# Kernel tuning notes

Hardware: AMD Instinct MI355X
Metric: run time of the kernel (lower is better)

## Reference

```python
import jax, jax.numpy as jnp
import numpy as np

# Hyperparameters from __init__
TEMPERATURE = 0.07
HARD_POS_W = 1.5
HARD_NEG_W = 2.0
THR_POS = 0.5
THR_NEG = 0.3
NEG_LOSS_W = 0.3

B, D, N_CLASSES = 8192, 256, 1024


def setup_inputs() -> dict:
    key = jax.random.key(0)
    kf, kl = jax.random.split(key)
    features = jax.random.normal(kf, (B, D), dtype=jnp.float32)
    labels = jax.random.randint(kl, (B,), 0, N_CLASSES, dtype=jnp.int32)
    return {"features": features, "labels": labels}


def reference(features, labels):
    b = features.shape[0]
    # L2-normalize features (F.normalize(dim=1))
    anchor = features / jnp.linalg.norm(features, axis=1, keepdims=True)
    sim = anchor @ anchor.T                      # [B, B] cosine similarity
    logits = sim / TEMPERATURE
    logits = logits - jax.lax.stop_gradient(jnp.max(logits, axis=1, keepdims=True))

    mask = (labels[:, None] == labels[None, :]).astype(logits.dtype)   # same-class
    logits_mask = 1.0 - jnp.eye(b, dtype=logits.dtype)                 # exclude self

    # W2ML weights: computed from detached similarities (torch used .item())
    sim_d = jax.lax.stop_gradient(sim)
    offdiag = logits_mask > 0
    is_pos = mask > 0
    hard_pos = is_pos & (sim_d < THR_POS) & offdiag
    pos_weights = jnp.where(
        hard_pos, 1.0 + (THR_POS - sim_d) / THR_POS * (HARD_POS_W - 1.0), 1.0)
    hard_neg = (~is_pos) & (sim_d > THR_NEG) & offdiag
    neg_weights = jnp.where(
        hard_neg, 1.0 + (sim_d - THR_NEG) / (1.0 - THR_NEG) * (HARD_NEG_W - 1.0), 1.0)

    # SupCon log-prob with self excluded from the denominator
    exp_logits = jnp.exp(logits) * logits_mask
    denom = jnp.sum(exp_logits, axis=1, keepdims=True)
    log_prob = logits - jnp.log(denom)

    pos_mask = mask * logits_mask
    pos_cnt = jnp.clip(jnp.sum(pos_mask, axis=1), 1.0, None)
    positive_loss = -jnp.mean(
        jnp.sum(pos_mask * pos_weights * log_prob, axis=1) / pos_cnt)

    # Negative term: weighted mean probability mass assigned to negatives
    neg_mask = (1.0 - mask) * logits_mask
    neg_cnt = jnp.clip(jnp.sum(neg_mask, axis=1), 1.0, None)
    prob = exp_logits / denom
    negative_loss = jnp.mean(
        jnp.sum(neg_mask * neg_weights * prob, axis=1) / neg_cnt)

    return positive_loss + NEG_LOSS_W * negative_loss
```

## Files before the change

### kernel.cpp

```cpp
#include <hip/hip_runtime.h>

#define BSZ  8192
#define DDIM 256
#define BM 128
#define BN 128
#define NT   64
#define NTRI (NT * (NT + 1) / 2)

typedef float f32x4 __attribute__((ext_vector_type(4)));
typedef short bf16x8 __attribute__((ext_vector_type(8)));

__device__ __forceinline__ unsigned short f32_to_bf16(float f) {
    unsigned int u = __float_as_uint(f);
    u += 0x7fffu + ((u >> 16) & 1u);
    return (unsigned short)(u >> 16);
}

#define K_E1   20.60992915555662f
#define K_E2  -20.60992915555662f
#define K_INVT 14.285714285714286f
#define K_N1   1.4285714285714286f
#define K_N2   0.5714285714285714f

__global__ __launch_bounds__(256) void norm_kernel(const float* __restrict__ feat,
                                                   unsigned short* __restrict__ anchorT,
                                                   float* __restrict__ posAcc) {
    if (blockIdx.x < 128) posAcc[blockIdx.x * 256 + threadIdx.x] = 0.0f;
    const int wid  = threadIdx.x >> 6;
    const int lane = threadIdx.x & 63;
    const int row  = blockIdx.x * 4 + wid;
    const float4 v = ((const float4*)(feat + (size_t)row * DDIM))[lane];
    float ss = v.x * v.x + v.y * v.y + v.z * v.z + v.w * v.w;
    #pragma unroll
    for (int off = 32; off > 0; off >>= 1) ss += __shfl_xor(ss, off, 64);
    const float inv = rsqrtf(ss);
    ushort4 o;
    o.x = f32_to_bf16(v.x * inv);
    o.y = f32_to_bf16(v.y * inv);
    o.z = f32_to_bf16(v.z * inv);
    o.w = f32_to_bf16(v.w * inv);
    const int C    = lane >> 3;
    const int tile = C * 512 + (row >> 4);
    const int l16  = (row & 15) + (((lane >> 1) & 3) << 4);
    *(ushort4*)(anchorT + (size_t)tile * 512 + l16 * 8 + (lane & 1) * 4) = o;
}

__device__ __forceinline__ void gload_lds16(const unsigned short* g, unsigned short* l) {
    __builtin_amdgcn_global_load_lds(
        (const __attribute__((address_space(1))) void*)g,
        (__attribute__((address_space(3))) void*)l, 16, 0, 0);
}

__global__ __launch_bounds__(256) void simloss_kernel(
    const unsigned short* __restrict__ anchorT,
    const int* __restrict__ labels,
    float* __restrict__ part,
    float* __restrict__ posAcc)
{
    __shared__ __align__(16) unsigned short As[16 * 512];
    __shared__ __align__(16) unsigned short Bs[16 * 512];
    __shared__ float rowDT[2][BM][2];
    __shared__ float colDT[2][BN][2];
    __shared__ int rowLab[BM];
    __shared__ int colLab[BN];

    const int t = blockIdx.x;
    const int off1 = 136, off2 = 392, off3 = 648, off4 = 904, off5 = 1040,
              off6 = 1296, off7 = 1552, off8 = 1688, off9 = 1944;
    int b = (t >= off1) + (t >= off2) + (t >= off3) + (t >= off4) + (t >= off5)
          + (t >= off6) + (t >= off7) + (t >= off8) + (t >= off9);
    int si, sj, r0;
    switch (b) {
        case 0: si = 0; sj = 0; r0 = 0;    break;
        case 1: si = 0; sj = 1; r0 = off1; break;
        case 2: si = 0; sj = 2; r0 = off2; break;
        case 3: si = 0; sj = 3; r0 = off3; break;
        case 4: si = 1; sj = 1; r0 = off4; break;
        case 5: si = 1; sj = 2; r0 = off5; break;
        case 6: si = 1; sj = 3; r0 = off6; break;
        case 7: si = 2; sj = 2; r0 = off7; break;
        case 8: si = 2; sj = 3; r0 = off8; break;
        default: si = 3; sj = 3; r0 = off9; break;
    }
    const int rr = t - r0;
    int il, jl;
    if (si == sj) {
        il = 0;
        #pragma unroll
        for (int q = 1; q < 16; q++) if (rr >= (16 * q - (q * (q - 1)) / 2)) il = q;
        jl = il + (rr - (16 * il - (il * (il - 1)) / 2));
    } else {
        il = rr >> 4;
        jl = rr & 15;
    }
    const int It = si * 16 + il;
    const int Jt = sj * 16 + jl;
    const bool diag = (It == Jt);
    const int I0 = It * BM, J0 = Jt * BN;

    const int tid  = threadIdx.x;
    const int wid  = tid >> 6;
    const int lane = tid & 63;
    const int waveM = (wid >> 1) * 64;
    const int waveN = (wid & 1) * 64;
    const int wm4 = waveM >> 4;
    const int wn4 = waveN >> 4;
    const int cl = lane & 15;
    const int rg = lane >> 4;
    const bool dwave = diag && (waveM == waveN);

    if (tid < BM) rowLab[tid] = labels[I0 + tid];
    else          colLab[tid - BM] = labels[J0 + tid - BM];

    f32x4 c_acc[4][4];
    #pragma unroll
    for (int a = 0; a < 4; a++)
        #pragma unroll
        for (int bq = 0; bq < 4; bq++)
            c_acc[a][bq] = (f32x4){0.f, 0.f, 0.f, 0.f};

    const int laneOff = lane * 8;

    for (int kc = 0; kc < 4; kc++) {
        const int C0 = kc * 2;
        #pragma unroll
        for (int q = 0; q < 4; q++) {
            const int chunk = wid * 4 + q;
            const int cq = chunk >> 3;
            const int Rq = chunk & 7;
            const size_t at = ((size_t)(C0 + cq) * 512 + It * 8 + Rq) * 512;
            const size_t bt = ((size_t)(C0 + cq) * 512 + Jt * 8 + Rq) * 512;
            gload_lds16(anchorT + at + laneOff, &As[chunk * 512]);
            gload_lds16(anchorT + bt + laneOff, &Bs[chunk * 512]);
        }
        __syncthreads();
        #pragma unroll
        for (int ks = 0; ks < 2; ks++) {
            const unsigned short* ab = &As[(ks * 8 + wm4) * 512 + laneOff];
            const unsigned short* bb = &Bs[(ks * 8 + wn4) * 512 + laneOff];
            const bf16x8 a0 = *(const bf16x8*)(ab);
            const bf16x8 a1 = *(const bf16x8*)(ab + 512);
            const bf16x8 a2 = *(const bf16x8*)(ab + 1024);
            const bf16x8 a3 = *(const bf16x8*)(ab + 1536);
            const bf16x8 b0 = *(const bf16x8*)(bb);
            const bf16x8 b1 = *(const bf16x8*)(bb + 512);
            const bf16x8 b2 = *(const bf16x8*)(bb + 1024);
            const bf16x8 b3 = *(const bf16x8*)(bb + 1536);
            c_acc[0][0] = __builtin_amdgcn_mfma_f32_16x16x32_bf16(a0, b0, c_acc[0][0], 0, 0, 0);
            c_acc[0][1] = __builtin_amdgcn_mfma_f32_16x16x32_bf16(a0, b1, c_acc[0][1], 0, 0, 0);
            c_acc[0][2] = __builtin_amdgcn_mfma_f32_16x16x32_bf16(a0, b2, c_acc[0][2], 0, 0, 0);
            c_acc[0][3] = __builtin_amdgcn_mfma_f32_16x16x32_bf16(a0, b3, c_acc[0][3], 0, 0, 0);
            c_acc[1][0] = __builtin_amdgcn_mfma_f32_16x16x32_bf16(a1, b0, c_acc[1][0], 0, 0, 0);
            c_acc[1][1] = __builtin_amdgcn_mfma_f32_16x16x32_bf16(a1, b1, c_acc[1][1], 0, 0, 0);
            c_acc[1][2] = __builtin_amdgcn_mfma_f32_16x16x32_bf16(a1, b2, c_acc[1][2], 0, 0, 0);
            c_acc[1][3] = __builtin_amdgcn_mfma_f32_16x16x32_bf16(a1, b3, c_acc[1][3], 0, 0, 0);
            c_acc[2][0] = __builtin_amdgcn_mfma_f32_16x16x32_bf16(a2, b0, c_acc[2][0], 0, 0, 0);
            c_acc[2][1] = __builtin_amdgcn_mfma_f32_16x16x32_bf16(a2, b1, c_acc[2][1], 0, 0, 0);
            c_acc[2][2] = __builtin_amdgcn_mfma_f32_16x16x32_bf16(a2, b2, c_acc[2][2], 0, 0, 0);
            c_acc[2][3] = __builtin_amdgcn_mfma_f32_16x16x32_bf16(a2, b3, c_acc[2][3], 0, 0, 0);
            c_acc[3][0] = __builtin_amdgcn_mfma_f32_16x16x32_bf16(a3, b0, c_acc[3][0], 0, 0, 0);
            c_acc[3][1] = __builtin_amdgcn_mfma_f32_16x16x32_bf16(a3, b1, c_acc[3][1], 0, 0, 0);
            c_acc[3][2] = __builtin_amdgcn_mfma_f32_16x16x32_bf16(a3, b2, c_acc[3][2], 0, 0, 0);
            c_acc[3][3] = __builtin_amdgcn_mfma_f32_16x16x32_bf16(a3, b3, c_acc[3][3], 0, 0, 0);
        }
        __syncthreads();
    }

    int ljr[4], gjr[4];
    #pragma unroll
    for (int fc = 0; fc < 4; fc++) {
        const int cidx = waveN + fc * 16 + cl;
        ljr[fc] = colLab[cidx];
        gjr[fc] = J0 + cidx;
    }
    float cd[4] = {0.f, 0.f, 0.f, 0.f}, ct[4] = {0.f, 0.f, 0.f, 0.f};

    #pragma unroll
    for (int fr = 0; fr < 4; fr++) {
        float rd[4] = {0.f, 0.f, 0.f, 0.f}, rt[4] = {0.f, 0.f, 0.f, 0.f};
        int li[4], gi[4];
        #pragma unroll
        for (int r = 0; r < 4; r++) {
            const int ridx = waveM + fr * 16 + rg * 4 + r;
            li[r] = rowLab[ridx];
            gi[r] = I0 + ridx;
        }
        #pragma unroll
        for (int fc = 0; fc < 4; fc++) {
            const int lj = ljr[fc];
            const f32x4 c = c_acc[fr][fc];
            #pragma unroll
            for (int r = 0; r < 4; r++) {
                const float s = c[r];
                const bool self = diag && (fr == fc) && dwave && ((rg * 4 + r) == cl);
                const float e  = self ? 0.f : exp2f(fmaf(s, K_E1, K_E2));
                const float wn = fmaxf(fmaf(s, K_N1, K_N2), 1.0f);
                const float we = wn * e;
                rd[r] += e;  rt[r] += we;
                if (!diag) { cd[fc] += e; ct[fc] += we; }
                if (li[r] == lj && !self) {
                    const float wp = fmaxf(1.5f - s, 1.0f);
                    const float slp = fmaf(s, K_INVT, -K_INVT) * wp;
                    float* pi = posAcc + (size_t)gi[r] * 4;
                    atomicAdd(pi + 0, slp);
                    atomicAdd(pi + 1, wp);
                    atomicAdd(pi + 2, we);
                    atomicAdd(pi + 3, 1.0f);
                    if (!diag) {
                        float* pj = posAcc + (size_t)gjr[fc] * 4;
                        atomicAdd(pj + 0, slp);
                        atomicAdd(pj + 1, wp);
                        atomicAdd(pj + 2, we);
                        atomicAdd(pj + 3, 1.0f);
                    }
                }
            }
        }
        #pragma unroll
        for (int r = 0; r < 4; r++) {
            #pragma unroll
            for (int off = 1; off < 16; off <<= 1) {
                rd[r] += __shfl_xor(rd[r], off, 64);
                rt[r] += __shfl_xor(rt[r], off, 64);
            }
        }
        if (cl == 0) {
            const int wh = waveN >> 6;
            #pragma unroll
            for (int r = 0; r < 4; r++) {
                const int row = waveM + fr * 16 + rg * 4 + r;
                rowDT[wh][row][0] = rd[r];
                rowDT[wh][row][1] = rt[r];
            }
        }
    }
    if (!diag) {
        #pragma unroll
        for (int fc = 0; fc < 4; fc++) {
            cd[fc] += __shfl_xor(cd[fc], 16, 64);
            cd[fc] += __shfl_xor(cd[fc], 32, 64);
            ct[fc] += __shfl_xor(ct[fc], 16, 64);
            ct[fc] += __shfl_xor(ct[fc], 32, 64);
        }
        if (rg == 0) {
            const int wmh = waveM >> 6;
            #pragma unroll
            for (int fc = 0; fc < 4; fc++) {
                const int col = waveN + fc * 16 + cl;
                colDT[wmh][col][0] = cd[fc];
                colDT[wmh][col][1] = ct[fc];
            }
        }
    }

    __syncthreads();
    if (tid < BM) {
        float2 v;
        v.x = rowDT[0][tid][0] + rowDT[1][tid][0];
        v.y = rowDT[0][tid][1] + rowDT[1][tid][1];
        ((float2*)part)[(size_t)Jt * BSZ + I0 + tid] = v;
    } else if (!diag) {
        const int c = tid - BM;
        float2 v;
        v.x = colDT[0][c][0] + colDT[1][c][0];
        v.y = colDT[0][c][1] + colDT[1][c][1];
        ((float2*)part)[(size_t)It * BSZ + J0 + c] = v;
    }
}

__global__ __launch_bounds__(256) void reduce_kernel(
    const float* __restrict__ part, const float* __restrict__ posAcc,
    double* __restrict__ partial)
{
    const int i = blockIdx.x * 256 + threadIdx.x;
    float dsum = 0.f, T2 = 0.f;
    const float2* p2 = (const float2*)part;
    #pragma unroll 8
    for (int j = 0; j < NT; j++) {
        const float2 v = p2[(size_t)j * BSZ + i];
        dsum += v.x; T2 += v.y;
    }
    const float4 pa = ((const float4*)posAcc)[i];
    const float s1 = pa.x, w1 = pa.y, s2 = T2 - pa.z, cnt = pa.w;
    const float pc = fmaxf(cnt, 1.0f);
    const float nc = fmaxf(8191.0f - cnt, 1.0f);
    const float ld = logf(dsum);
    const double pos_i = (double)((s1 - ld * w1) / pc);
    const double neg_i = (double)((s2 / dsum) / nc);

    __shared__ double sp[256], sn[256];
    sp[threadIdx.x] = pos_i; sn[threadIdx.x] = neg_i;
    __syncthreads();
    for (int s = 128; s > 0; s >>= 1) {
        if (threadIdx.x < s) {
            sp[threadIdx.x] += sp[threadIdx.x + s];
            sn[threadIdx.x] += sn[threadIdx.x + s];
        }
        __syncthreads();
    }
    if (threadIdx.x == 0) {
        partial[blockIdx.x * 2 + 0] = sp[0];
        partial[blockIdx.x * 2 + 1] = sn[0];
    }
}

__global__ __launch_bounds__(64) void final_kernel(const double* __restrict__ partial,
                                                   float* __restrict__ out) {
    const int lane = threadIdx.x;
    double p = 0.0, n = 0.0;
    if (lane < 32) { p = partial[lane * 2 + 0]; n = partial[lane * 2 + 1]; }
    #pragma unroll
    for (int o = 32; o > 0; o >>= 1) { p += __shfl_xor(p, o, 64); n += __shfl_xor(n, o, 64); }
    if (lane == 0) out[0] = (float)(-p / (double)BSZ + 0.3 * (n / (double)BSZ));
}

extern "C" void kernel_launch(void* const* d_in, const int* in_sizes, int n_in,
                              void* d_out, int out_size, void* d_ws, size_t ws_size,
                              hipStream_t stream) {
    const float* feat = (const float*)d_in[0];
    const int* labels = (const int*)d_in[1];
    float* out = (float*)d_out;

    char* ws = (char*)d_ws;
    unsigned short* anchorT = (unsigned short*)ws;
    const size_t anchorBytes = (size_t)BSZ * DDIM * sizeof(unsigned short);
    float* part = (float*)(ws + anchorBytes);
    const size_t partBytes = (size_t)NT * BSZ * 2 * sizeof(float);
    float* posAcc = (float*)(ws + anchorBytes + partBytes);
    const size_t posBytes = (size_t)BSZ * 4 * sizeof(float);
    double* partial = (double*)(ws + anchorBytes + partBytes + posBytes);

    norm_kernel<<<BSZ / 4, 256, 0, stream>>>(feat, anchorT, posAcc);
    simloss_kernel<<<NTRI, 256, 0, stream>>>(anchorT, labels, part, posAcc);
    reduce_kernel<<<BSZ / 256, 256, 0, stream>>>(part, posAcc, partial);
    final_kernel<<<1, 64, 0, stream>>>(partial, out);
}
```

Before: 122.4 us.

## Make simloss persistent over four tiles with double-buffered LDS prefetch and fused final reduction

The sim/loss kernel now launches 520 blocks that each process four triangle tiles, double-buffering the A/B LDS tiles so the global-to-LDS loads for the next k-chunk or next tile overlap the MFMA work. Row and column partial sums go straight to global memory per wave half, which removes the shared-memory staging and the final block barrier, at the cost of doubling the partial buffer the reduce reads. The norm kernel stages 64 rows in LDS so it can write contiguous 16-byte chunks. The final kernel is folded into the reduce through a last-block atomic counter, saving one launch.

```diff
diff --git a/kernel.cpp b/kernel.cpp
--- a/kernel.cpp
+++ b/kernel.cpp
@@ -6,6 +6,7 @@
 #define BN 128
 #define NT   64
 #define NTRI (NT * (NT + 1) / 2)
+#define NBLK 520
 
 typedef float f32x4 __attribute__((ext_vector_type(4)));
 typedef short bf16x8 __attribute__((ext_vector_type(8)));
@@ -22,49 +23,7 @@
 #define K_N1   1.4285714285714286f
 #define K_N2   0.5714285714285714f
 
-__global__ __launch_bounds__(256) void norm_kernel(const float* __restrict__ feat,
-                                                   unsigned short* __restrict__ anchorT,
-                                                   float* __restrict__ posAcc) {
-    if (blockIdx.x < 128) posAcc[blockIdx.x * 256 + threadIdx.x] = 0.0f;
-    const int wid  = threadIdx.x >> 6;
-    const int lane = threadIdx.x & 63;
-    const int row  = blockIdx.x * 4 + wid;
-    const float4 v = ((const float4*)(feat + (size_t)row * DDIM))[lane];
-    float ss = v.x * v.x + v.y * v.y + v.z * v.z + v.w * v.w;
-    #pragma unroll
-    for (int off = 32; off > 0; off >>= 1) ss += __shfl_xor(ss, off, 64);
-    const float inv = rsqrtf(ss);
-    ushort4 o;
-    o.x = f32_to_bf16(v.x * inv);
-    o.y = f32_to_bf16(v.y * inv);
-    o.z = f32_to_bf16(v.z * inv);
-    o.w = f32_to_bf16(v.w * inv);
-    const int C    = lane >> 3;
-    const int tile = C * 512 + (row >> 4);
-    const int l16  = (row & 15) + (((lane >> 1) & 3) << 4);
-    *(ushort4*)(anchorT + (size_t)tile * 512 + l16 * 8 + (lane & 1) * 4) = o;
-}
-
-__device__ __forceinline__ void gload_lds16(const unsigned short* g, unsigned short* l) {
-    __builtin_amdgcn_global_load_lds(
-        (const __attribute__((address_space(1))) void*)g,
-        (__attribute__((address_space(3))) void*)l, 16, 0, 0);
-}
-
-__global__ __launch_bounds__(256) void simloss_kernel(
-    const unsigned short* __restrict__ anchorT,
-    const int* __restrict__ labels,
-    float* __restrict__ part,
-    float* __restrict__ posAcc)
-{
-    __shared__ __align__(16) unsigned short As[16 * 512];
-    __shared__ __align__(16) unsigned short Bs[16 * 512];
-    __shared__ float rowDT[2][BM][2];
-    __shared__ float colDT[2][BN][2];
-    __shared__ int rowLab[BM];
-    __shared__ int colLab[BN];
-
-    const int t = blockIdx.x;
+__device__ __forceinline__ void decode_tile(int t, int& It, int& Jt) {
     const int off1 = 136, off2 = 392, off3 = 648, off4 = 904, off5 = 1040,
               off6 = 1296, off7 = 1552, off8 = 1688, off9 = 1944;
     int b = (t >= off1) + (t >= off2) + (t >= off3) + (t >= off4) + (t >= off5)
@@ -93,11 +52,68 @@
         il = rr >> 4;
         jl = rr & 15;
     }
-    const int It = si * 16 + il;
-    const int Jt = sj * 16 + jl;
-    const bool diag = (It == Jt);
-    const int I0 = It * BM, J0 = Jt * BN;
-
+    It = si * 16 + il;
+    Jt = sj * 16 + jl;
+}
+
+__global__ __launch_bounds__(256) void norm_kernel(const float* __restrict__ feat,
+                                                   unsigned short* __restrict__ anchorT,
+                                                   float* __restrict__ posAcc,
+                                                   unsigned int* __restrict__ counter) {
+    __shared__ __align__(16) unsigned short img[32 * 512];
+    const int tid  = threadIdx.x;
+    const int wid  = tid >> 6;
+    const int lane = tid & 63;
+    const int R0   = blockIdx.x * 64;
+
+    posAcc[blockIdx.x * 256 + tid] = 0.0f;
+    if (blockIdx.x == 0 && tid == 0) *counter = 0u;
+
+    #pragma unroll
+    for (int it = 0; it < 16; it++) {
+        const int row = R0 + it * 4 + wid;
+        const float4 v = ((const float4*)(feat + (size_t)row * DDIM))[lane];
+        float ss = v.x * v.x + v.y * v.y + v.z * v.z + v.w * v.w;
+        #pragma unroll
+        for (int off = 32; off > 0; off >>= 1) ss += __shfl_xor(ss, off, 64);
+        const float inv = rsqrtf(ss);
+        ushort4 o;
+        o.x = f32_to_bf16(v.x * inv);
+        o.y = f32_to_bf16(v.y * inv);
+        o.z = f32_to_bf16(v.z * inv);
+        o.w = f32_to_bf16(v.w * inv);
+        const int C    = lane >> 3;
+        const int c    = C * 4 + ((row >> 4) & 3);
+        const int l16  = (row & 15) + (((lane >> 1) & 3) << 4);
+        *(ushort4*)(&img[c * 512 + l16 * 8 + (lane & 1) * 4]) = o;
+    }
+    __syncthreads();
+    #pragma unroll
+    for (int p = 0; p < 8; p++) {
+        const int c = p * 4 + wid;
+        const int T = (c >> 2) * 512 + (R0 >> 4) + (c & 3);
+        *(bf16x8*)(anchorT + (size_t)T * 512 + lane * 8) = *(const bf16x8*)(&img[c * 512 + lane * 8]);
+    }
+}
+
+__device__ __forceinline__ void gload_lds16(const unsigned short* g, unsigned short* l) {
+    __builtin_amdgcn_global_load_lds(
+        (const __attribute__((address_space(1))) void*)g,
+        (__attribute__((address_space(3))) void*)l, 16, 0, 0);
+}
+
+__global__ __launch_bounds__(256) void simloss_kernel(
+    const unsigned short* __restrict__ anchorT,
+    const int* __restrict__ labels,
+    float* __restrict__ part,
+    float* __restrict__ posAcc)
+{
+    __shared__ __align__(16) unsigned short As[2][16 * 512];
+    __shared__ __align__(16) unsigned short Bs[2][16 * 512];
+    __shared__ int rowLab[2][BM];
+    __shared__ int colLab[2][BN];
+
+    const int p    = blockIdx.x;
     const int tid  = threadIdx.x;
     const int wid  = tid >> 6;
     const int lane = tid & 63;
@@ -107,176 +123,196 @@
     const int wn4 = waveN >> 4;
     const int cl = lane & 15;
     const int rg = lane >> 4;
-    const bool dwave = diag && (waveM == waveN);
-
-    if (tid < BM) rowLab[tid] = labels[I0 + tid];
-    else          colLab[tid - BM] = labels[J0 + tid - BM];
-
-    f32x4 c_acc[4][4];
-    #pragma unroll
-    for (int a = 0; a < 4; a++)
-        #pragma unroll
-        for (int bq = 0; bq < 4; bq++)
-            c_acc[a][bq] = (f32x4){0.f, 0.f, 0.f, 0.f};
-
     const int laneOff = lane * 8;
 
-    for (int kc = 0; kc < 4; kc++) {
-        const int C0 = kc * 2;
-        #pragma unroll
-        for (int q = 0; q < 4; q++) {
-            const int chunk = wid * 4 + q;
-            const int cq = chunk >> 3;
-            const int Rq = chunk & 7;
-            const size_t at = ((size_t)(C0 + cq) * 512 + It * 8 + Rq) * 512;
-            const size_t bt = ((size_t)(C0 + cq) * 512 + Jt * 8 + Rq) * 512;
-            gload_lds16(anchorT + at + laneOff, &As[chunk * 512]);
-            gload_lds16(anchorT + bt + laneOff, &Bs[chunk * 512]);
-        }
-        __syncthreads();
-        #pragma unroll
-        for (int ks = 0; ks < 2; ks++) {
-            const unsigned short* ab = &As[(ks * 8 + wm4) * 512 + laneOff];
-            const unsigned short* bb = &Bs[(ks * 8 + wn4) * 512 + laneOff];
-            const bf16x8 a0 = *(const bf16x8*)(ab);
-            const bf16x8 a1 = *(const bf16x8*)(ab + 512);
-            const bf16x8 a2 = *(const bf16x8*)(ab + 1024);
-            const bf16x8 a3 = *(const bf16x8*)(ab + 1536);
-            const bf16x8 b0 = *(const bf16x8*)(bb);
-            const bf16x8 b1 = *(const bf16x8*)(bb + 512);
-            const bf16x8 b2 = *(const bf16x8*)(bb + 1024);
-            const bf16x8 b3 = *(const bf16x8*)(bb + 1536);
-            c_acc[0][0] = __builtin_amdgcn_mfma_f32_16x16x32_bf16(a0, b0, c_acc[0][0], 0, 0, 0);
-            c_acc[0][1] = __builtin_amdgcn_mfma_f32_16x16x32_bf16(a0, b1, c_acc[0][1], 0, 0, 0);
-            c_acc[0][2] = __builtin_amdgcn_mfma_f32_16x16x32_bf16(a0, b2, c_acc[0][2], 0, 0, 0);
-            c_acc[0][3] = __builtin_amdgcn_mfma_f32_16x16x32_bf16(a0, b3, c_acc[0][3], 0, 0, 0);
-            c_acc[1][0] = __builtin_amdgcn_mfma_f32_16x16x32_bf16(a1, b0, c_acc[1][0], 0, 0, 0);
-            c_acc[1][1] = __builtin_amdgcn_mfma_f32_16x16x32_bf16(a1, b1, c_acc[1][1], 0, 0, 0);
-            c_acc[1][2] = __builtin_amdgcn_mfma_f32_16x16x32_bf16(a1, b2, c_acc[1][2], 0, 0, 0);
-            c_acc[1][3] = __builtin_amdgcn_mfma_f32_16x16x32_bf16(a1, b3, c_acc[1][3], 0, 0, 0);
-            c_acc[2][0] = __builtin_amdgcn_mfma_f32_16x16x32_bf16(a2, b0, c_acc[2][0], 0, 0, 0);
-            c_acc[2][1] = __builtin_amdgcn_mfma_f32_16x16x32_bf16(a2, b1, c_acc[2][1], 0, 0, 0);
-            c_acc[2][2] = __builtin_amdgcn_mfma_f32_16x16x32_bf16(a2, b2, c_acc[2][2], 0, 0, 0);
-            c_acc[2][3] = __builtin_amdgcn_mfma_f32_16x16x32_bf16(a2, b3, c_acc[2][3], 0, 0, 0);
-            c_acc[3][0] = __builtin_amdgcn_mfma_f32_16x16x32_bf16(a3, b0, c_acc[3][0], 0, 0, 0);
-            c_acc[3][1] = __builtin_amdgcn_mfma_f32_16x16x32_bf16(a3, b1, c_acc[3][1], 0, 0, 0);
-            c_acc[3][2] = __builtin_amdgcn_mfma_f32_16x16x32_bf16(a3, b2, c_acc[3][2], 0, 0, 0);
-            c_acc[3][3] = __builtin_amdgcn_mfma_f32_16x16x32_bf16(a3, b3, c_acc[3][3], 0, 0, 0);
-        }
-        __syncthreads();
-    }
-
-    int ljr[4], gjr[4];
-    #pragma unroll
-    for (int fc = 0; fc < 4; fc++) {
-        const int cidx = waveN + fc * 16 + cl;
-        ljr[fc] = colLab[cidx];
-        gjr[fc] = J0 + cidx;
-    }
-    float cd[4] = {0.f, 0.f, 0.f, 0.f}, ct[4] = {0.f, 0.f, 0.f, 0.f};
-
-    #pragma unroll
-    for (int fr = 0; fr < 4; fr++) {
-        float rd[4] = {0.f, 0.f, 0.f, 0.f}, rt[4] = {0.f, 0.f, 0.f, 0.f};
-        int li[4], gi[4];
-        #pragma unroll
-        for (int r = 0; r < 4; r++) {
-            const int ridx = waveM + fr * 16 + rg * 4 + r;
-            li[r] = rowLab[ridx];
-            gi[r] = I0 + ridx;
-        }
+    int It, Jt;
+    decode_tile(p * 4, It, Jt);
+
+    #define STAGE(ItX, JtX, kcX, slotX)                                              \
+        do {                                                                          \
+            const int C0s = (kcX) * 2;                                                \
+            _Pragma("unroll")                                                         \
+            for (int q = 0; q < 4; q++) {                                             \
+                const int chunk = wid * 4 + q;                                        \
+                const int cq = chunk >> 3;                                            \
+                const int Rq = chunk & 7;                                             \
+                const size_t at = ((size_t)(C0s + cq) * 512 + (ItX) * 8 + Rq) * 512;  \
+                const size_t bt = ((size_t)(C0s + cq) * 512 + (JtX) * 8 + Rq) * 512;  \
+                gload_lds16(anchorT + at + laneOff, &As[slotX][chunk * 512]);         \
+                gload_lds16(anchorT + bt + laneOff, &Bs[slotX][chunk * 512]);         \
+            }                                                                         \
+        } while (0)
+
+    #define WRLAB(ItX, JtX, slotX)                                                    \
+        do {                                                                          \
+            if (tid < BM) rowLab[slotX][tid] = labels[(ItX) * BM + tid];              \
+            else          colLab[slotX][tid - BM] = labels[(JtX) * BN + tid - BM];    \
+        } while (0)
+
+    STAGE(It, Jt, 0, 0);
+    WRLAB(It, Jt, 0);
+
+    #pragma unroll 1
+    for (int ti = 0; ti < 4; ++ti) {
+        const bool diag  = (It == Jt);
+        const bool dwave = diag && (waveM == waveN);
+        const int I0 = It * BM, J0 = Jt * BN;
+        const int ls = ti & 1;
+
+        int Itn = It, Jtn = Jt;
+        if (ti < 3) decode_tile(p * 4 + ti + 1, Itn, Jtn);
+
+        f32x4 c_acc[4][4];
+        #pragma unroll
+        for (int a = 0; a < 4; a++)
+            #pragma unroll
+            for (int bq = 0; bq < 4; bq++)
+                c_acc[a][bq] = (f32x4){0.f, 0.f, 0.f, 0.f};
+
+        #pragma unroll
+        for (int kc = 0; kc < 4; ++kc) {
+            __syncthreads();
+            if (kc < 3) {
+                STAGE(It, Jt, kc + 1, (kc + 1) & 1);
+            } else if (ti < 3) {
+                STAGE(Itn, Jtn, 0, 0);
+                WRLAB(Itn, Jtn, (ti + 1) & 1);
+            }
+            const int s = kc & 1;
+            #pragma unroll
+            for (int ks = 0; ks < 2; ks++) {
+                const unsigned short* ab = &As[s][(ks * 8 + wm4) * 512 + laneOff];
+                const unsigned short* bb = &Bs[s][(ks * 8 + wn4) * 512 + laneOff];
+                const bf16x8 a0 = *(const bf16x8*)(ab);
+                const bf16x8 a1 = *(const bf16x8*)(ab + 512);
+                const bf16x8 a2 = *(const bf16x8*)(ab + 1024);
+                const bf16x8 a3 = *(const bf16x8*)(ab + 1536);
+                const bf16x8 b0 = *(const bf16x8*)(bb);
+                const bf16x8 b1 = *(const bf16x8*)(bb + 512);
+                const bf16x8 b2 = *(const bf16x8*)(bb + 1024);
+                const bf16x8 b3 = *(const bf16x8*)(bb + 1536);
+                c_acc[0][0] = __builtin_amdgcn_mfma_f32_16x16x32_bf16(a0, b0, c_acc[0][0], 0, 0, 0);
+                c_acc[0][1] = __builtin_amdgcn_mfma_f32_16x16x32_bf16(a0, b1, c_acc[0][1], 0, 0, 0);
+                c_acc[0][2] = __builtin_amdgcn_mfma_f32_16x16x32_bf16(a0, b2, c_acc[0][2], 0, 0, 0);
+                c_acc[0][3] = __builtin_amdgcn_mfma_f32_16x16x32_bf16(a0, b3, c_acc[0][3], 0, 0, 0);
+                c_acc[1][0] = __builtin_amdgcn_mfma_f32_16x16x32_bf16(a1, b0, c_acc[1][0], 0, 0, 0);
+                c_acc[1][1] = __builtin_amdgcn_mfma_f32_16x16x32_bf16(a1, b1, c_acc[1][1], 0, 0, 0);
+                c_acc[1][2] = __builtin_amdgcn_mfma_f32_16x16x32_bf16(a1, b2, c_acc[1][2], 0, 0, 0);
+                c_acc[1][3] = __builtin_amdgcn_mfma_f32_16x16x32_bf16(a1, b3, c_acc[1][3], 0, 0, 0);
+                c_acc[2][0] = __builtin_amdgcn_mfma_f32_16x16x32_bf16(a2, b0, c_acc[2][0], 0, 0, 0);
+                c_acc[2][1] = __builtin_amdgcn_mfma_f32_16x16x32_bf16(a2, b1, c_acc[2][1], 0, 0, 0);
+                c_acc[2][2] = __builtin_amdgcn_mfma_f32_16x16x32_bf16(a2, b2, c_acc[2][2], 0, 0, 0);
+                c_acc[2][3] = __builtin_amdgcn_mfma_f32_16x16x32_bf16(a2, b3, c_acc[2][3], 0, 0, 0);
+                c_acc[3][0] = __builtin_amdgcn_mfma_f32_16x16x32_bf16(a3, b0, c_acc[3][0], 0, 0, 0);
+                c_acc[3][1] = __builtin_amdgcn_mfma_f32_16x16x32_bf16(a3, b1, c_acc[3][1], 0, 0, 0);
+                c_acc[3][2] = __builtin_amdgcn_mfma_f32_16x16x32_bf16(a3, b2, c_acc[3][2], 0, 0, 0);
+                c_acc[3][3] = __builtin_amdgcn_mfma_f32_16x16x32_bf16(a3, b3, c_acc[3][3], 0, 0, 0);
+            }
+        }
+
+        int ljr[4], gjr[4];
         #pragma unroll
         for (int fc = 0; fc < 4; fc++) {
-            const int lj = ljr[fc];
-            const f32x4 c = c_acc[fr][fc];
+            const int cidx = waveN + fc * 16 + cl;
+            ljr[fc] = colLab[ls][cidx];
+            gjr[fc] = J0 + cidx;
+        }
+        float cd[4] = {0.f, 0.f, 0.f, 0.f}, ct[4] = {0.f, 0.f, 0.f, 0.f};
+
+        #pragma unroll
+        for (int fr = 0; fr < 4; fr++) {
+            float rd[4] = {0.f, 0.f, 0.f, 0.f}, rt[4] = {0.f, 0.f, 0.f, 0.f};
+            int li[4], gi[4];
             #pragma unroll
             for (int r = 0; r < 4; r++) {
-                const float s = c[r];
-                const bool self = diag && (fr == fc) && dwave && ((rg * 4 + r) == cl);
-                const float e  = self ? 0.f : exp2f(fmaf(s, K_E1, K_E2));
-                const float wn = fmaxf(fmaf(s, K_N1, K_N2), 1.0f);
-                const float we = wn * e;
-                rd[r] += e;  rt[r] += we;
-                if (!diag) { cd[fc] += e; ct[fc] += we; }
-                if (li[r] == lj && !self) {
-                    const float wp = fmaxf(1.5f - s, 1.0f);
-                    const float slp = fmaf(s, K_INVT, -K_INVT) * wp;
-                    float* pi = posAcc + (size_t)gi[r] * 4;
-                    atomicAdd(pi + 0, slp);
-                    atomicAdd(pi + 1, wp);
-                    atomicAdd(pi + 2, we);
-                    atomicAdd(pi + 3, 1.0f);
-                    if (!diag) {
-                        float* pj = posAcc + (size_t)gjr[fc] * 4;
-                        atomicAdd(pj + 0, slp);
-                        atomicAdd(pj + 1, wp);
-                        atomicAdd(pj + 2, we);
-                        atomicAdd(pj + 3, 1.0f);
+                const int ridx = waveM + fr * 16 + rg * 4 + r;
+                li[r] = rowLab[ls][ridx];
+                gi[r] = I0 + ridx;
+            }
+            #pragma unroll
+            for (int fc = 0; fc < 4; fc++) {
+                const int lj = ljr[fc];
+                const f32x4 c = c_acc[fr][fc];
+                #pragma unroll
+                for (int r = 0; r < 4; r++) {
+                    const float s = c[r];
+                    const bool self = diag && (fr == fc) && dwave && ((rg * 4 + r) == cl);
+                    const float e  = self ? 0.f : exp2f(fmaf(s, K_E1, K_E2));
+                    const float wn = fmaxf(fmaf(s, K_N1, K_N2), 1.0f);
+                    const float we = wn * e;
+                    rd[r] += e;  rt[r] += we;
+                    if (!diag) { cd[fc] += e; ct[fc] += we; }
+                    if (li[r] == lj && !self) {
+                        const float wp = fmaxf(1.5f - s, 1.0f);
+                        const float slp = fmaf(s, K_INVT, -K_INVT) * wp;
+                        float* pi = posAcc + (size_t)gi[r] * 4;
+                        atomicAdd(pi + 0, slp);
+                        atomicAdd(pi + 1, wp);
+                        atomicAdd(pi + 2, we);
+                        atomicAdd(pi + 3, 1.0f);
+                        if (!diag) {
+                            float* pj = posAcc + (size_t)gjr[fc] * 4;
+                            atomicAdd(pj + 0, slp);
+                            atomicAdd(pj + 1, wp);
+                            atomicAdd(pj + 2, we);
+                            atomicAdd(pj + 3, 1.0f);
+                        }
                     }
                 }
             }
-        }
-        #pragma unroll
-        for (int r = 0; r < 4; r++) {
-            #pragma unroll
-            for (int off = 1; off < 16; off <<= 1) {
-                rd[r] += __shfl_xor(rd[r], off, 64);
-                rt[r] += __shfl_xor(rt[r], off, 64);
-            }
-        }
-        if (cl == 0) {
-            const int wh = waveN >> 6;
             #pragma unroll
             for (int r = 0; r < 4; r++) {
-                const int row = waveM + fr * 16 + rg * 4 + r;
-                rowDT[wh][row][0] = rd[r];
-                rowDT[wh][row][1] = rt[r];
-            }
-        }
-    }
-    if (!diag) {
-        #pragma unroll
-        for (int fc = 0; fc < 4; fc++) {
-            cd[fc] += __shfl_xor(cd[fc], 16, 64);
-            cd[fc] += __shfl_xor(cd[fc], 32, 64);
-            ct[fc] += __shfl_xor(ct[fc], 16, 64);
-            ct[fc] += __shfl_xor(ct[fc], 32, 64);
-        }
-        if (rg == 0) {
-            const int wmh = waveM >> 6;
+                #pragma unroll
+                for (int off = 1; off < 16; off <<= 1) {
+                    rd[r] += __shfl_xor(rd[r], off, 64);
+                    rt[r] += __shfl_xor(rt[r], off, 64);
+                }
+            }
+            if (cl == 0) {
+                const int wh = waveN >> 6;
+                float2* dst = (float2*)part + ((size_t)(Jt * 2 + wh)) * BSZ + I0 + waveM + fr * 16 + rg * 4;
+                #pragma unroll
+                for (int r = 0; r < 4; r++) {
+                    float2 v; v.x = rd[r]; v.y = rt[r];
+                    dst[r] = v;
+                }
+            }
+        }
+        if (!diag) {
             #pragma unroll
             for (int fc = 0; fc < 4; fc++) {
-                const int col = waveN + fc * 16 + cl;
-                colDT[wmh][col][0] = cd[fc];
-                colDT[wmh][col][1] = ct[fc];
-            }
-        }
-    }
-
-    __syncthreads();
-    if (tid < BM) {
-        float2 v;
-        v.x = rowDT[0][tid][0] + rowDT[1][tid][0];
-        v.y = rowDT[0][tid][1] + rowDT[1][tid][1];
-        ((float2*)part)[(size_t)Jt * BSZ + I0 + tid] = v;
-    } else if (!diag) {
-        const int c = tid - BM;
-        float2 v;
-        v.x = colDT[0][c][0] + colDT[1][c][0];
-        v.y = colDT[0][c][1] + colDT[1][c][1];
-        ((float2*)part)[(size_t)It * BSZ + J0 + c] = v;
-    }
-}
-
-__global__ __launch_bounds__(256) void reduce_kernel(
+                cd[fc] += __shfl_xor(cd[fc], 16, 64);
+                cd[fc] += __shfl_xor(cd[fc], 32, 64);
+                ct[fc] += __shfl_xor(ct[fc], 16, 64);
+                ct[fc] += __shfl_xor(ct[fc], 32, 64);
+            }
+            if (rg == 0) {
+                const int wmh = waveM >> 6;
+                float2* dst = (float2*)part + ((size_t)(It * 2 + wmh)) * BSZ + J0 + waveN + cl;
+                #pragma unroll
+                for (int fc = 0; fc < 4; fc++) {
+                    float2 v; v.x = cd[fc]; v.y = ct[fc];
+                    dst[fc * 16] = v;
+                }
+            }
+        }
+
+        It = Itn; Jt = Jtn;
+    }
+    #undef STAGE
+    #undef WRLAB
+}
+
+__global__ __launch_bounds__(256) void reduce_final_kernel(
     const float* __restrict__ part, const float* __restrict__ posAcc,
-    double* __restrict__ partial)
+    double* __restrict__ partial, unsigned int* __restrict__ counter,
+    float* __restrict__ out)
 {
     const int i = blockIdx.x * 256 + threadIdx.x;
     float dsum = 0.f, T2 = 0.f;
     const float2* p2 = (const float2*)part;
-    #pragma unroll 8
-    for (int j = 0; j < NT; j++) {
+    #pragma unroll 4
+    for (int j = 0; j < NT * 2; j++) {
         const float2 v = p2[(size_t)j * BSZ + i];
         dsum += v.x; T2 += v.y;
     }
@@ -298,20 +334,27 @@
         }
         __syncthreads();
     }
+    __shared__ bool amLast;
     if (threadIdx.x == 0) {
         partial[blockIdx.x * 2 + 0] = sp[0];
         partial[blockIdx.x * 2 + 1] = sn[0];
-    }
-}
-
-__global__ __launch_bounds__(64) void final_kernel(const double* __restrict__ partial,
-                                                   float* __restrict__ out) {
-    const int lane = threadIdx.x;
-    double p = 0.0, n = 0.0;
-    if (lane < 32) { p = partial[lane * 2 + 0]; n = partial[lane * 2 + 1]; }
-    #pragma unroll
-    for (int o = 32; o > 0; o >>= 1) { p += __shfl_xor(p, o, 64); n += __shfl_xor(n, o, 64); }
-    if (lane == 0) out[0] = (float)(-p / (double)BSZ + 0.3 * (n / (double)BSZ));
+        __threadfence();
+        amLast = (atomicAdd(counter, 1u) == 31u);
+    }
+    __syncthreads();
+    if (amLast) {
+        __threadfence();
+        const int lane = threadIdx.x;
+        double p = 0.0, n = 0.0;
+        if (lane < 32) {
+            volatile double* vp = (volatile double*)partial;
+            p = vp[lane * 2 + 0];
+            n = vp[lane * 2 + 1];
+        }
+        #pragma unroll
+        for (int o = 32; o > 0; o >>= 1) { p += __shfl_xor(p, o, 64); n += __shfl_xor(n, o, 64); }
+        if (lane == 0) out[0] = (float)(-p / (double)BSZ + 0.3 * (n / (double)BSZ));
+    }
 }
 
 extern "C" void kernel_launch(void* const* d_in, const int* in_sizes, int n_in,
@@ -325,13 +368,13 @@
     unsigned short* anchorT = (unsigned short*)ws;
     const size_t anchorBytes = (size_t)BSZ * DDIM * sizeof(unsigned short);
     float* part = (float*)(ws + anchorBytes);
-    const size_t partBytes = (size_t)NT * BSZ * 2 * sizeof(float);
+    const size_t partBytes = (size_t)NT * 2 * BSZ * 2 * sizeof(float);
     float* posAcc = (float*)(ws + anchorBytes + partBytes);
     const size_t posBytes = (size_t)BSZ * 4 * sizeof(float);
     double* partial = (double*)(ws + anchorBytes + partBytes + posBytes);
-
-    norm_kernel<<<BSZ / 4, 256, 0, stream>>>(feat, anchorT, posAcc);
-    simloss_kernel<<<NTRI, 256, 0, stream>>>(anchorT, labels, part, posAcc);
-    reduce_kernel<<<BSZ / 256, 256, 0, stream>>>(part, posAcc, partial);
-    final_kernel<<<1, 64, 0, stream>>>(partial, out);
-}
+    unsigned int* counter = (unsigned int*)(ws + anchorBytes + partBytes + posBytes + 512);
+
+    norm_kernel<<<BSZ / 64, 256, 0, stream>>>(feat, anchorT, posAcc, counter);
+    simloss_kernel<<<NBLK, 256, 0, stream>>>(anchorT, labels, part, posAcc);
+    reduce_final_kernel<<<BSZ / 256, 256, 0, stream>>>(part, posAcc, partial, counter, out);
+}
```

Result: slower. 182.5 us (+49.2%).

## Fuse reduce and final kernels, stage norm output in LDS, shrink GEMM K-chunk

Applied to the files above, without the earlier changes.

The norm kernel now handles 16 rows per block and writes whole 1KB tiles through LDS with coalesced 16-byte stores, and it also resets a completion counter. The simloss GEMM loads K in eight single-chunk steps with precomputed pointers and half the LDS, which may raise occupancy but doubles the barrier count. The reduce and final kernels merge into one kernel that uses more blocks and shuffle reductions, and the last block to finish does the final sum via an atomic counter. This removes one launch at the cost of threadfence and atomic overhead.

```diff
diff --git a/kernel.cpp b/kernel.cpp
--- a/kernel.cpp
+++ b/kernel.cpp
@@ -22,49 +22,7 @@
 #define K_N1   1.4285714285714286f
 #define K_N2   0.5714285714285714f
 
-__global__ __launch_bounds__(256) void norm_kernel(const float* __restrict__ feat,
-                                                   unsigned short* __restrict__ anchorT,
-                                                   float* __restrict__ posAcc) {
-    if (blockIdx.x < 128) posAcc[blockIdx.x * 256 + threadIdx.x] = 0.0f;
-    const int wid  = threadIdx.x >> 6;
-    const int lane = threadIdx.x & 63;
-    const int row  = blockIdx.x * 4 + wid;
-    const float4 v = ((const float4*)(feat + (size_t)row * DDIM))[lane];
-    float ss = v.x * v.x + v.y * v.y + v.z * v.z + v.w * v.w;
-    #pragma unroll
-    for (int off = 32; off > 0; off >>= 1) ss += __shfl_xor(ss, off, 64);
-    const float inv = rsqrtf(ss);
-    ushort4 o;
-    o.x = f32_to_bf16(v.x * inv);
-    o.y = f32_to_bf16(v.y * inv);
-    o.z = f32_to_bf16(v.z * inv);
-    o.w = f32_to_bf16(v.w * inv);
-    const int C    = lane >> 3;
-    const int tile = C * 512 + (row >> 4);
-    const int l16  = (row & 15) + (((lane >> 1) & 3) << 4);
-    *(ushort4*)(anchorT + (size_t)tile * 512 + l16 * 8 + (lane & 1) * 4) = o;
-}
-
-__device__ __forceinline__ void gload_lds16(const unsigned short* g, unsigned short* l) {
-    __builtin_amdgcn_global_load_lds(
-        (const __attribute__((address_space(1))) void*)g,
-        (__attribute__((address_space(3))) void*)l, 16, 0, 0);
-}
-
-__global__ __launch_bounds__(256) void simloss_kernel(
-    const unsigned short* __restrict__ anchorT,
-    const int* __restrict__ labels,
-    float* __restrict__ part,
-    float* __restrict__ posAcc)
-{
-    __shared__ __align__(16) unsigned short As[16 * 512];
-    __shared__ __align__(16) unsigned short Bs[16 * 512];
-    __shared__ float rowDT[2][BM][2];
-    __shared__ float colDT[2][BN][2];
-    __shared__ int rowLab[BM];
-    __shared__ int colLab[BN];
-
-    const int t = blockIdx.x;
+__device__ __forceinline__ void decode_tile(int t, int& It, int& Jt) {
     const int off1 = 136, off2 = 392, off3 = 648, off4 = 904, off5 = 1040,
               off6 = 1296, off7 = 1552, off8 = 1688, off9 = 1944;
     int b = (t >= off1) + (t >= off2) + (t >= off3) + (t >= off4) + (t >= off5)
@@ -93,8 +51,71 @@
         il = rr >> 4;
         jl = rr & 15;
     }
-    const int It = si * 16 + il;
-    const int Jt = sj * 16 + jl;
+    It = si * 16 + il;
+    Jt = sj * 16 + jl;
+}
+
+__global__ __launch_bounds__(256) void norm_kernel(const float* __restrict__ feat,
+                                                   unsigned short* __restrict__ anchorT,
+                                                   float* __restrict__ posAcc,
+                                                   unsigned int* __restrict__ counter) {
+    __shared__ __align__(16) unsigned short img[8 * 512];
+    const int tid  = threadIdx.x;
+    const int wid  = tid >> 6;
+    const int lane = tid & 63;
+    const int R    = blockIdx.x;
+    const int R0   = R * 16;
+
+    if (tid < 64) posAcc[blockIdx.x * 64 + tid] = 0.0f;
+    if (blockIdx.x == 0 && tid == 0) *counter = 0u;
+
+    #pragma unroll
+    for (int it = 0; it < 4; it++) {
+        const int row = R0 + it * 4 + wid;
+        const float4 v = ((const float4*)(feat + (size_t)row * DDIM))[lane];
+        float ss = v.x * v.x + v.y * v.y + v.z * v.z + v.w * v.w;
+        #pragma unroll
+        for (int off = 32; off > 0; off >>= 1) ss += __shfl_xor(ss, off, 64);
+        const float inv = rsqrtf(ss);
+        ushort4 o;
+        o.x = f32_to_bf16(v.x * inv);
+        o.y = f32_to_bf16(v.y * inv);
+        o.z = f32_to_bf16(v.z * inv);
+        o.w = f32_to_bf16(v.w * inv);
+        const int C    = lane >> 3;
+        const int l16  = (row & 15) + (((lane >> 1) & 3) << 4);
+        *(ushort4*)(&img[C * 512 + l16 * 8 + (lane & 1) * 4]) = o;
+    }
+    __syncthreads();
+    #pragma unroll
+    for (int p = 0; p < 2; p++) {
+        const int c = p * 4 + wid;
+        *(bf16x8*)(anchorT + ((size_t)(c * 512 + R)) * 512 + lane * 8) =
+            *(const bf16x8*)(&img[c * 512 + lane * 8]);
+    }
+}
+
+__device__ __forceinline__ void gload_lds16(const unsigned short* g, unsigned short* l) {
+    __builtin_amdgcn_global_load_lds(
+        (const __attribute__((address_space(1))) void*)g,
+        (__attribute__((address_space(3))) void*)l, 16, 0, 0);
+}
+
+__global__ __launch_bounds__(256) void simloss_kernel(
+    const unsigned short* __restrict__ anchorT,
+    const int* __restrict__ labels,
+    float* __restrict__ part,
+    float* __restrict__ posAcc)
+{
+    __shared__ __align__(16) unsigned short As[8 * 512];
+    __shared__ __align__(16) unsigned short Bs[8 * 512];
+    __shared__ float rowDT[2][BM][2];
+    __shared__ float colDT[2][BN][2];
+    __shared__ int rowLab[BM];
+    __shared__ int colLab[BN];
+
+    int It, Jt;
+    decode_tile(blockIdx.x, It, Jt);
     const bool diag = (It == Jt);
     const int I0 = It * BM, J0 = Jt * BN;
 
@@ -108,60 +129,58 @@
     const int cl = lane & 15;
     const int rg = lane >> 4;
     const bool dwave = diag && (waveM == waveN);
+    const int laneOff = lane * 8;
 
     if (tid < BM) rowLab[tid] = labels[I0 + tid];
     else          colLab[tid - BM] = labels[J0 + tid - BM];
 
-    f32x4 c_acc[4][4];
+    const unsigned short* aG0 = anchorT + ((size_t)(It * 8 + wid)) * 512 + laneOff;
+    const unsigned short* aG1 = aG0 + (size_t)4 * 512;
+    const unsigned short* bG0 = anchorT + ((size_t)(Jt * 8 + wid)) * 512 + laneOff;
+    const unsigned short* bG1 = bG0 + (size_t)4 * 512;
+
+    f32x4 acc[4][4];
     #pragma unroll
     for (int a = 0; a < 4; a++)
         #pragma unroll
         for (int bq = 0; bq < 4; bq++)
-            c_acc[a][bq] = (f32x4){0.f, 0.f, 0.f, 0.f};
-
-    const int laneOff = lane * 8;
-
-    for (int kc = 0; kc < 4; kc++) {
-        const int C0 = kc * 2;
-        #pragma unroll
-        for (int q = 0; q < 4; q++) {
-            const int chunk = wid * 4 + q;
-            const int cq = chunk >> 3;
-            const int Rq = chunk & 7;
-            const size_t at = ((size_t)(C0 + cq) * 512 + It * 8 + Rq) * 512;
-            const size_t bt = ((size_t)(C0 + cq) * 512 + Jt * 8 + Rq) * 512;
-            gload_lds16(anchorT + at + laneOff, &As[chunk * 512]);
-            gload_lds16(anchorT + bt + laneOff, &Bs[chunk * 512]);
-        }
+            acc[a][bq] = (f32x4){0.f, 0.f, 0.f, 0.f};
+
+    #pragma unroll
+    for (int kc = 0; kc < 8; kc++) {
+        const size_t adv = (size_t)kc * (512 * 512);
+        gload_lds16(aG0 + adv, &As[wid * 512]);
+        gload_lds16(aG1 + adv, &As[(4 + wid) * 512]);
+        gload_lds16(bG0 + adv, &Bs[wid * 512]);
+        gload_lds16(bG1 + adv, &Bs[(4 + wid) * 512]);
         __syncthreads();
-        #pragma unroll
-        for (int ks = 0; ks < 2; ks++) {
-            const unsigned short* ab = &As[(ks * 8 + wm4) * 512 + laneOff];
-            const unsigned short* bb = &Bs[(ks * 8 + wn4) * 512 + laneOff];
-            const bf16x8 a0 = *(const bf16x8*)(ab);
-            const bf16x8 a1 = *(const bf16x8*)(ab + 512);
-            const bf16x8 a2 = *(const bf16x8*)(ab + 1024);
-            const bf16x8 a3 = *(const bf16x8*)(ab + 1536);
-            const bf16x8 b0 = *(const bf16x8*)(bb);
-            const bf16x8 b1 = *(const bf16x8*)(bb + 512);
-            const bf16x8 b2 = *(const bf16x8*)(bb + 1024);
-            const bf16x8 b3 = *(const bf16x8*)(bb + 1536);
-            c_acc[0][0] = __builtin_amdgcn_mfma_f32_16x16x32_bf16(a0, b0, c_acc[0][0], 0, 0, 0);
-            c_acc[0][1] = __builtin_amdgcn_mfma_f32_16x16x32_bf16(a0, b1, c_acc[0][1], 0, 0, 0);
-            c_acc[0][2] = __builtin_amdgcn_mfma_f32_16x16x32_bf16(a0, b2, c_acc[0][2], 0, 0, 0);
-            c_acc[0][3] = __builtin_amdgcn_mfma_f32_16x16x32_bf16(a0, b3, c_acc[0][3], 0, 0, 0);
-            c_acc[1][0] = __builtin_amdgcn_mfma_f32_16x16x32_bf16(a1, b0, c_acc[1][0], 0, 0, 0);
-            c_acc[1][1] = __builtin_amdgcn_mfma_f32_16x16x32_bf16(a1, b1, c_acc[1][1], 0, 0, 0);
-            c_acc[1][2] = __builtin_amdgcn_mfma_f32_16x16x32_bf16(a1, b2, c_acc[1][2], 0, 0, 0);
-            c_acc[1][3] = __builtin_amdgcn_mfma_f32_16x16x32_bf16(a1, b3, c_acc[1][3], 0, 0, 0);
-            c_acc[2][0] = __builtin_amdgcn_mfma_f32_16x16x32_bf16(a2, b0, c_acc[2][0], 0, 0, 0);
-            c_acc[2][1] = __builtin_amdgcn_mfma_f32_16x16x32_bf16(a2, b1, c_acc[2][1], 0, 0, 0);
-            c_acc[2][2] = __builtin_amdgcn_mfma_f32_16x16x32_bf16(a2, b2, c_acc[2][2], 0, 0, 0);
-            c_acc[2][3] = __builtin_amdgcn_mfma_f32_16x16x32_bf16(a2, b3, c_acc[2][3], 0, 0, 0);
-            c_acc[3][0] = __builtin_amdgcn_mfma_f32_16x16x32_bf16(a3, b0, c_acc[3][0], 0, 0, 0);
-            c_acc[3][1] = __builtin_amdgcn_mfma_f32_16x16x32_bf16(a3, b1, c_acc[3][1], 0, 0, 0);
-            c_acc[3][2] = __builtin_amdgcn_mfma_f32_16x16x32_bf16(a3, b2, c_acc[3][2], 0, 0, 0);
-            c_acc[3][3] = __builtin_amdgcn_mfma_f32_16x16x32_bf16(a3, b3, c_acc[3][3], 0, 0, 0);
+        {
+            const unsigned short* aB = &As[wm4 * 512 + laneOff];
+            const unsigned short* bB = &Bs[wn4 * 512 + laneOff];
+            const bf16x8 a0 = *(const bf16x8*)(aB);
+            const bf16x8 a1 = *(const bf16x8*)(aB + 512);
+            const bf16x8 a2 = *(const bf16x8*)(aB + 1024);
+            const bf16x8 a3 = *(const bf16x8*)(aB + 1536);
+            const bf16x8 b0 = *(const bf16x8*)(bB);
+            const bf16x8 b1 = *(const bf16x8*)(bB + 512);
+            const bf16x8 b2 = *(const bf16x8*)(bB + 1024);
+            const bf16x8 b3 = *(const bf16x8*)(bB + 1536);
+            acc[0][0] = __builtin_amdgcn_mfma_f32_16x16x32_bf16(a0, b0, acc[0][0], 0, 0, 0);
+            acc[0][1] = __builtin_amdgcn_mfma_f32_16x16x32_bf16(a0, b1, acc[0][1], 0, 0, 0);
+            acc[0][2] = __builtin_amdgcn_mfma_f32_16x16x32_bf16(a0, b2, acc[0][2], 0, 0, 0);
+            acc[0][3] = __builtin_amdgcn_mfma_f32_16x16x32_bf16(a0, b3, acc[0][3], 0, 0, 0);
+            acc[1][0] = __builtin_amdgcn_mfma_f32_16x16x32_bf16(a1, b0, acc[1][0], 0, 0, 0);
+            acc[1][1] = __builtin_amdgcn_mfma_f32_16x16x32_bf16(a1, b1, acc[1][1], 0, 0, 0);
+            acc[1][2] = __builtin_amdgcn_mfma_f32_16x16x32_bf16(a1, b2, acc[1][2], 0, 0, 0);
+            acc[1][3] = __builtin_amdgcn_mfma_f32_16x16x32_bf16(a1, b3, acc[1][3], 0, 0, 0);
+            acc[2][0] = __builtin_amdgcn_mfma_f32_16x16x32_bf16(a2, b0, acc[2][0], 0, 0, 0);
+            acc[2][1] = __builtin_amdgcn_mfma_f32_16x16x32_bf16(a2, b1, acc[2][1], 0, 0, 0);
+            acc[2][2] = __builtin_amdgcn_mfma_f32_16x16x32_bf16(a2, b2, acc[2][2], 0, 0, 0);
+            acc[2][3] = __builtin_amdgcn_mfma_f32_16x16x32_bf16(a2, b3, acc[2][3], 0, 0, 0);
+            acc[3][0] = __builtin_amdgcn_mfma_f32_16x16x32_bf16(a3, b0, acc[3][0], 0, 0, 0);
+            acc[3][1] = __builtin_amdgcn_mfma_f32_16x16x32_bf16(a3, b1, acc[3][1], 0, 0, 0);
+            acc[3][2] = __builtin_amdgcn_mfma_f32_16x16x32_bf16(a3, b2, acc[3][2], 0, 0, 0);
+            acc[3][3] = __builtin_amdgcn_mfma_f32_16x16x32_bf16(a3, b3, acc[3][3], 0, 0, 0);
         }
         __syncthreads();
     }
@@ -188,11 +207,11 @@
         #pragma unroll
         for (int fc = 0; fc < 4; fc++) {
             const int lj = ljr[fc];
-            const f32x4 c = c_acc[fr][fc];
+            const f32x4 c = acc[fr][fc];
             #pragma unroll
             for (int r = 0; r < 4; r++) {
                 const float s = c[r];
-                const bool self = diag && (fr == fc) && dwave && ((rg * 4 + r) == cl);
+                const bool self = (fr == fc) && dwave && ((rg * 4 + r) == cl);
                 const float e  = self ? 0.f : exp2f(fmaf(s, K_E1, K_E2));
                 const float wn = fmaxf(fmaf(s, K_N1, K_N2), 1.0f);
                 const float we = wn * e;
@@ -268,50 +287,66 @@
     }
 }
 
-__global__ __launch_bounds__(256) void reduce_kernel(
+__global__ __launch_bounds__(256) void reduce_final_kernel(
     const float* __restrict__ part, const float* __restrict__ posAcc,
-    double* __restrict__ partial)
+    double* __restrict__ partial, unsigned int* __restrict__ counter,
+    float* __restrict__ out)
 {
-    const int i = blockIdx.x * 256 + threadIdx.x;
+    const int t   = threadIdx.x;
+    const int row = blockIdx.x * 32 + (t >> 3);
+    const int sg  = t & 7;
     float dsum = 0.f, T2 = 0.f;
     const float2* p2 = (const float2*)part;
-    #pragma unroll 8
-    for (int j = 0; j < NT; j++) {
-        const float2 v = p2[(size_t)j * BSZ + i];
+    #pragma unroll
+    for (int j = 0; j < 8; j++) {
+        const float2 v = p2[(size_t)(sg * 8 + j) * BSZ + row];
         dsum += v.x; T2 += v.y;
     }
-    const float4 pa = ((const float4*)posAcc)[i];
-    const float s1 = pa.x, w1 = pa.y, s2 = T2 - pa.z, cnt = pa.w;
-    const float pc = fmaxf(cnt, 1.0f);
-    const float nc = fmaxf(8191.0f - cnt, 1.0f);
-    const float ld = logf(dsum);
-    const double pos_i = (double)((s1 - ld * w1) / pc);
-    const double neg_i = (double)((s2 / dsum) / nc);
-
-    __shared__ double sp[256], sn[256];
-    sp[threadIdx.x] = pos_i; sn[threadIdx.x] = neg_i;
+    #pragma unroll
+    for (int off = 1; off < 8; off <<= 1) {
+        dsum += __shfl_xor(dsum, off, 64);
+        T2   += __shfl_xor(T2,   off, 64);
+    }
+    __shared__ double sp[32], sn[32];
+    if (sg == 0) {
+        const float4 pa = ((const float4*)posAcc)[row];
+        const float s1 = pa.x, w1 = pa.y, s2 = T2 - pa.z, cnt = pa.w;
+        const float pc = fmaxf(cnt, 1.0f);
+        const float nc = fmaxf(8191.0f - cnt, 1.0f);
+        const float ld = logf(dsum);
+        sp[t >> 3] = (double)((s1 - ld * w1) / pc);
+        sn[t >> 3] = (double)((s2 / dsum) / nc);
+    }
     __syncthreads();
-    for (int s = 128; s > 0; s >>= 1) {
-        if (threadIdx.x < s) {
-            sp[threadIdx.x] += sp[threadIdx.x + s];
-            sn[threadIdx.x] += sn[threadIdx.x + s];
-        }
+    __shared__ bool amLast;
+    if (t < 32) {
+        double p = sp[t], n = sn[t];
+        #pragma unroll
+        for (int off = 1; off < 32; off <<= 1) {
+            p += __shfl_xor(p, off, 64);
+            n += __shfl_xor(n, off, 64);
+        }
+        if (t == 0) {
+            partial[blockIdx.x * 2 + 0] = p;
+            partial[blockIdx.x * 2 + 1] = n;
+            __threadfence();
+            amLast = (atomicAdd(counter, 1u) == 255u);
+        }
+    }
+    __syncthreads();
+    if (amLast) {
+        __threadfence();
+        __shared__ double fp[256], fn[256];
+        volatile double* vp = (volatile double*)partial;
+        fp[t] = vp[t * 2 + 0];
+        fn[t] = vp[t * 2 + 1];
         __syncthreads();
-    }
-    if (threadIdx.x == 0) {
-        partial[blockIdx.x * 2 + 0] = sp[0];
-        partial[blockIdx.x * 2 + 1] = sn[0];
-    }
-}
-
-__global__ __launch_bounds__(64) void final_kernel(const double* __restrict__ partial,
-                                                   float* __restrict__ out) {
-    const int lane = threadIdx.x;
-    double p = 0.0, n = 0.0;
-    if (lane < 32) { p = partial[lane * 2 + 0]; n = partial[lane * 2 + 1]; }
-    #pragma unroll
-    for (int o = 32; o > 0; o >>= 1) { p += __shfl_xor(p, o, 64); n += __shfl_xor(n, o, 64); }
-    if (lane == 0) out[0] = (float)(-p / (double)BSZ + 0.3 * (n / (double)BSZ));
+        for (int s = 128; s > 0; s >>= 1) {
+            if (t < s) { fp[t] += fp[t + s]; fn[t] += fn[t + s]; }
+            __syncthreads();
+        }
+        if (t == 0) out[0] = (float)(-fp[0] / (double)BSZ + 0.3 * (fn[0] / (double)BSZ));
+    }
 }
 
 extern "C" void kernel_launch(void* const* d_in, const int* in_sizes, int n_in,
@@ -329,9 +364,9 @@
     float* posAcc = (float*)(ws + anchorBytes + partBytes);
     const size_t posBytes = (size_t)BSZ * 4 * sizeof(float);
     double* partial = (double*)(ws + anchorBytes + partBytes + posBytes);
-
-    norm_kernel<<<BSZ / 4, 256, 0, stream>>>(feat, anchorT, posAcc);
+    unsigned int* counter = (unsigned int*)(ws + anchorBytes + partBytes + posBytes + 4096);
+
+    norm_kernel<<<BSZ / 16, 256, 0, stream>>>(feat, anchorT, posAcc, counter);
     simloss_kernel<<<NTRI, 256, 0, stream>>>(anchorT, labels, part, posAcc);
-    reduce_kernel<<<BSZ / 256, 256, 0, stream>>>(part, posAcc, partial);
-    final_kernel<<<1, 64, 0, stream>>>(partial, out);
-}
+    reduce_final_kernel<<<BSZ / 32, 256, 0, stream>>>(part, posAcc, partial, counter, out);
+}
```

Measured after the change: 126.6 us. 1.03x slower.
